# Optimization experiments

Hardware: AMD Instinct MI355X
Metric: run time of the kernel (lower is better)

Reference implementation:

```python
import jax, jax.numpy as jnp
import numpy as np
import math

CHANNELS = 512
OUT_CHANNELS = 512
N_HEADS = 8
WINDOW = 4
K_CH = CHANNELS // N_HEADS


def _conv1x1(x, W, b):
    # x: (B, C_in, T), W: (C_out, C_in), b: (C_out,)
    return jnp.einsum('oc,bct->bot', W, x) + b[None, :, None]


def _get_relative_embeddings(emb, length, window=WINDOW):
    # emb: (H, 2*window+1, k_ch) -> (H, 2*length-1, k_ch)
    pad_length = max(length - (window + 1), 0)
    start = max(window + 1 - length, 0)
    e = jnp.pad(emb, ((0, 0), (pad_length, pad_length), (0, 0))) if pad_length > 0 else emb
    return e[:, start:start + 2 * length - 1]


def _relative_to_absolute(x):
    # x: (B, H, L, 2L-1) -> (B, H, L, L)
    b, h, L, _ = x.shape
    x = jnp.pad(x, ((0, 0), (0, 0), (0, 0), (0, 1)))          # (B,H,L,2L)
    xf = x.reshape(b, h, L * 2 * L)
    xf = jnp.pad(xf, ((0, 0), (0, 0), (L - 1, 0)))
    return xf.reshape(b, h, L + 1, 2 * L - 1)[:, :, :L, L - 1:]


def _absolute_to_relative(x):
    # x: (B, H, L, L) -> (B, H, L, 2L-1)
    b, h, L, _ = x.shape
    x = jnp.pad(x, ((0, 0), (0, 0), (0, 0), (0, L - 1)))       # (B,H,L,2L-1)
    xf = x.reshape(b, h, L * (2 * L - 1))
    xf = jnp.pad(xf, ((0, 0), (0, 0), (L, 0)))
    return xf.reshape(b, h, L, 2 * L)[:, :, :, 1:]


def setup_inputs() -> dict:
    key = jax.random.key(0)
    ks = jax.random.split(key, 16)
    B, C, T = 4, CHANNELS, 1024
    xavier = math.sqrt(2.0 / (C + C))
    rel_std = K_CH ** -0.5
    return {
        'x_q': jax.random.normal(ks[0], (B, C, T), jnp.float32),
        'x_k': jax.random.normal(ks[1], (B, C, T), jnp.float32),
        'x_v': jax.random.normal(ks[2], (B, C, T), jnp.float32),
        'Wq': jax.random.normal(ks[3], (C, C), jnp.float32) * xavier,
        'bq': jnp.zeros((C,), jnp.float32),
        'Wk': jax.random.normal(ks[4], (C, C), jnp.float32) * xavier,
        'bk': jnp.zeros((C,), jnp.float32),
        'Wv': jax.random.normal(ks[5], (C, C), jnp.float32) * xavier,
        'bv': jnp.zeros((C,), jnp.float32),
        'Wo': jax.random.normal(ks[6], (OUT_CHANNELS, C), jnp.float32) * xavier,
        'bo': jnp.zeros((OUT_CHANNELS,), jnp.float32),
        'emb_rel_k': jax.random.normal(ks[7], (N_HEADS, 2 * WINDOW + 1, K_CH), jnp.float32) * rel_std,
        'emb_rel_v': jax.random.normal(ks[8], (N_HEADS, 2 * WINDOW + 1, K_CH), jnp.float32) * rel_std,
    }


def reference(x_q, x_k, x_v, Wq, bq, Wk, bk, Wv, bv, Wo, bo, emb_rel_k, emb_rel_v):
    q = _conv1x1(x_q, Wq, bq)
    k = _conv1x1(x_k, Wk, bk)
    v = _conv1x1(x_v, Wv, bv)
    B, C, T = q.shape
    # (B, C, T) -> (B, H, T, k_ch); head h owns contiguous k_ch channel chunk
    qh = q.reshape(B, N_HEADS, K_CH, T).transpose(0, 1, 3, 2) / math.sqrt(K_CH)
    kh = k.reshape(B, N_HEADS, K_CH, T).transpose(0, 1, 3, 2)
    vh = v.reshape(B, N_HEADS, K_CH, T).transpose(0, 1, 3, 2)
    scores = jnp.einsum('bhtd,bhsd->bhts', qh, kh)              # (B,H,T,T)
    rel_k = _get_relative_embeddings(emb_rel_k, T)              # (H,2T-1,d)
    rel_logits = jnp.einsum('bhtd,hmd->bhtm', qh, rel_k)        # (B,H,T,2T-1)
    scores = scores + _relative_to_absolute(rel_logits)
    attn = jax.nn.softmax(scores, axis=-1)
    ctx = jnp.einsum('bhts,bhsd->bhtd', attn, vh)
    rel_w = _absolute_to_relative(attn)                         # (B,H,T,2T-1)
    rel_v = _get_relative_embeddings(emb_rel_v, T)
    ctx = ctx + jnp.einsum('bhtm,hmd->bhtd', rel_w, rel_v)
    out = ctx.transpose(0, 1, 3, 2).reshape(B, C, T)
    return _conv1x1(out, Wo, bo)
```

## Files before the change

kernel.cpp:

```cpp
#include <hip/hip_runtime.h>

#define T_LEN 1024
#define NH 8
#define DH 64
#define CCH 512
#define LOG2E 1.44269504088896340736f

typedef _Float16 f16;
typedef _Float16 f16x8 __attribute__((ext_vector_type(8)));
typedef _Float16 f16x4 __attribute__((ext_vector_type(4)));
typedef float f32x4 __attribute__((ext_vector_type(4)));

__global__ __launch_bounds__(256)
void xpose_fp16(const float* __restrict__ x0, const float* __restrict__ x1,
                const float* __restrict__ x2, f16* __restrict__ o0,
                f16* __restrict__ o1, f16* __restrict__ o2, int B)
{
    const int t0 = blockIdx.x * 64, c0 = blockIdx.y * 64;
    const int which = blockIdx.z / B, b = blockIdx.z % B;
    const float* x = (which == 0) ? x0 : (which == 1) ? x1 : x2;
    f16* o = (which == 0) ? o0 : (which == 1) ? o1 : o2;

    __shared__ float L[64 * 68];
    const int cl = threadIdx.x & 63, g = threadIdx.x >> 6;
    const float* src = x + ((size_t)(b * CCH + c0 + cl)) * T_LEN + t0 + g * 16;
    #pragma unroll
    for (int j = 0; j < 4; ++j)
        *(float4*)&L[cl * 68 + g * 16 + 4 * j] = *(const float4*)&src[4 * j];
    __syncthreads();
    const int tl = threadIdx.x & 63, cg = (threadIdx.x >> 6) * 16;
    f16 h[16];
    #pragma unroll
    for (int j = 0; j < 16; ++j) h[j] = (f16)L[(cg + j) * 68 + tl];
    f16* dst = o + ((size_t)(b * T_LEN + t0 + tl)) * CCH + c0 + cg;
    *(f16x8*)&dst[0] = *(f16x8*)&h[0];
    *(f16x8*)&dst[8] = *(f16x8*)&h[8];
}

__global__ __launch_bounds__(256)
void wconv(const float* __restrict__ w0, const float* __restrict__ w1,
           const float* __restrict__ w2, const float* __restrict__ w3,
           f16* __restrict__ o0, f16* __restrict__ o1,
           f16* __restrict__ o2, f16* __restrict__ o3)
{
    const int y = blockIdx.y;
    const float* w = (y == 0) ? w0 : (y == 1) ? w1 : (y == 2) ? w2 : w3;
    f16* o = (y == 0) ? o0 : (y == 1) ? o1 : (y == 2) ? o2 : o3;
    const int i = (blockIdx.x * 256 + threadIdx.x) * 4;
    float4 v = *(const float4*)&w[i];
    f16x4 hv = {(f16)v.x, (f16)v.y, (f16)v.z, (f16)v.w};
    *(f16x4*)&o[i] = hv;
}

__global__ __launch_bounds__(256)
void proj_qkv(const f16* __restrict__ xq, const f16* __restrict__ xk,
              const f16* __restrict__ xv, const f16* __restrict__ wq,
              const f16* __restrict__ wk, const f16* __restrict__ wv,
              const float* __restrict__ bq, const float* __restrict__ bk,
              const float* __restrict__ bv, f16* __restrict__ qo,
              f16* __restrict__ ko, f16* __restrict__ vo)
{
    const int which = blockIdx.z;
    const f16* X = (which == 0) ? xq : (which == 1) ? xk : xv;
    const f16* W = (which == 0) ? wq : (which == 1) ? wk : wv;
    const float* bias = (which == 0) ? bq : (which == 1) ? bk : bv;
    const float scale = (which == 0) ? 0.125f * LOG2E : 1.0f;

    const int r0 = blockIdx.x * 64;
    const int o0 = blockIdx.y * 64;
    const int tid = threadIdx.x;
    const int w = tid >> 6, quad = (tid >> 4) & 3, l15 = tid & 15;

    __shared__ f16 Xs[64 * 72], Ws[64 * 72];
    f32x4 acc[4] = {};

    for (int c0 = 0; c0 < CCH; c0 += 64) {
        if (c0) __syncthreads();
        #pragma unroll
        for (int j = 0; j < 2; ++j) {
            int cid = tid + 256 * j;
            int row = cid >> 3, c8 = (cid & 7) * 8;
            *(f16x8*)&Xs[row * 72 + c8] = *(const f16x8*)&X[(size_t)(r0 + row) * CCH + c0 + c8];
            *(f16x8*)&Ws[row * 72 + c8] = *(const f16x8*)&W[(size_t)(o0 + row) * CCH + c0 + c8];
        }
        __syncthreads();
        const f16* Ab = (which < 2) ? Xs : Ws;
        const f16* Bb = (which < 2) ? Ws : Xs;
        #pragma unroll
        for (int ks = 0; ks < 2; ++ks) {
            f16x8 a = *(const f16x8*)&Ab[(16 * w + l15) * 72 + ks * 32 + quad * 8];
            #pragma unroll
            for (int ct = 0; ct < 4; ++ct) {
                f16x8 bf = *(const f16x8*)&Bb[(16 * ct + l15) * 72 + ks * 32 + quad * 8];
                acc[ct] = __builtin_amdgcn_mfma_f32_16x16x32_f16(a, bf, acc[ct], 0, 0, 0);
            }
        }
    }

    if (which < 2) {
        f16* out = (which == 0) ? qo : ko;
        #pragma unroll
        for (int ct = 0; ct < 4; ++ct) {
            int col = o0 + 16 * ct + l15;
            float bvl = bias[col];
            #pragma unroll
            for (int r = 0; r < 4; ++r) {
                int row = r0 + 16 * w + quad * 4 + r;
                out[(size_t)row * CCH + col] = (f16)((acc[ct][r] + bvl) * scale);
            }
        }
    } else {
        const int bb = r0 >> 10, tb = r0 & 1023;
        #pragma unroll
        for (int r = 0; r < 4; ++r) {
            int row_o = o0 + 16 * w + quad * 4 + r;
            float bvl = bias[row_o];
            #pragma unroll
            for (int ct = 0; ct < 4; ++ct)
                vo[((size_t)(bb * CCH + row_o)) * T_LEN + tb + 16 * ct + l15] =
                    (f16)(acc[ct][r] + bvl);
        }
    }
}

__global__ __launch_bounds__(256)
void proj_out(const f16* __restrict__ ctx, const f16* __restrict__ Wo,
              const float* __restrict__ bo, float* __restrict__ out)
{
    const int r0 = blockIdx.x * 64;
    const int o0 = blockIdx.y * 64;
    const int tid = threadIdx.x;
    const int w = tid >> 6, quad = (tid >> 4) & 3, l15 = tid & 15;

    __shared__ f16 Xs[64 * 72], Ws[64 * 72];
    f32x4 acc[4] = {};

    for (int c0 = 0; c0 < CCH; c0 += 64) {
        if (c0) __syncthreads();
        #pragma unroll
        for (int j = 0; j < 2; ++j) {
            int cid = tid + 256 * j;
            int row = cid >> 3, c8 = (cid & 7) * 8;
            *(f16x8*)&Xs[row * 72 + c8] = *(const f16x8*)&ctx[(size_t)(r0 + row) * CCH + c0 + c8];
            *(f16x8*)&Ws[row * 72 + c8] = *(const f16x8*)&Wo[(size_t)(o0 + row) * CCH + c0 + c8];
        }
        __syncthreads();
        #pragma unroll
        for (int ks = 0; ks < 2; ++ks) {
            f16x8 a = *(const f16x8*)&Ws[(16 * w + l15) * 72 + ks * 32 + quad * 8];
            #pragma unroll
            for (int ct = 0; ct < 4; ++ct) {
                f16x8 bf = *(const f16x8*)&Xs[(16 * ct + l15) * 72 + ks * 32 + quad * 8];
                acc[ct] = __builtin_amdgcn_mfma_f32_16x16x32_f16(a, bf, acc[ct], 0, 0, 0);
            }
        }
    }

    const int bb = r0 >> 10, tb = r0 & 1023;
    #pragma unroll
    for (int r = 0; r < 4; ++r) {
        int row_o = o0 + 16 * w + quad * 4 + r;
        float bvl = bo[row_o];
        #pragma unroll
        for (int ct = 0; ct < 4; ++ct)
            out[((size_t)(bb * CCH + row_o)) * T_LEN + tb + 16 * ct + l15] =
                acc[ct][r] + bvl;
    }
}

__global__ __launch_bounds__(256)
void attn_mfma(const f16* __restrict__ q, const f16* __restrict__ k,
               const f16* __restrict__ v, const float* __restrict__ ekg,
               const float* __restrict__ evg, f16* __restrict__ ctx)
{
    const int t0 = blockIdx.x * 64, h = blockIdx.y, b = blockIdx.z;
    const int tid = threadIdx.x;
    const int w = tid >> 6, quad = (tid >> 4) & 3, l15 = tid & 15;

    __shared__ f16 Qs[64 * 72], Ks[64 * 72], Vs[64 * 72], Ps[64 * 72];
    __shared__ float eks[9 * 64], evs[9 * 64];

    for (int i = tid; i < 9 * 64; i += 256) {
        eks[i] = ekg[h * 9 * 64 + i];
        evs[i] = evg[h * 9 * 64 + i];
    }
    #pragma unroll
    for (int j = 0; j < 2; ++j) {
        int cid = tid + 256 * j;
        int row = cid >> 3, c8 = (cid & 7) * 8;
        *(f16x8*)&Qs[row * 72 + c8] =
            *(const f16x8*)&q[((size_t)(b * T_LEN + t0 + row)) * CCH + h * DH + c8];
    }
    __syncthreads();

    float m_run[4], l_run[4];
    f32x4 O[4] = {};
    #pragma unroll
    for (int r = 0; r < 4; ++r) { m_run[r] = -1e30f; l_run[r] = 0.f; }

    const bool corner_hi = (blockIdx.x == 0);
    const bool corner_lo = (blockIdx.x == 15);

    for (int kb = 0; kb < 16; ++kb) {
        const int s0 = kb * 64;
        if (kb) __syncthreads();
        #pragma unroll
        for (int j = 0; j < 2; ++j) {
            int cid = tid + 256 * j;
            int row = cid >> 3, c8 = (cid & 7) * 8;
            *(f16x8*)&Ks[row * 72 + c8] =
                *(const f16x8*)&k[((size_t)(b * T_LEN + s0 + row)) * CCH + h * DH + c8];
            *(f16x8*)&Vs[row * 72 + c8] =
                *(const f16x8*)&v[((size_t)(b * CCH + h * DH + row)) * T_LEN + s0 + c8];
        }
        __syncthreads();

        f32x4 S[4] = {};
        #pragma unroll
        for (int ks = 0; ks < 2; ++ks) {
            f16x8 a = *(const f16x8*)&Qs[(16 * w + l15) * 72 + ks * 32 + quad * 8];
            #pragma unroll
            for (int ct = 0; ct < 4; ++ct) {
                f16x8 bf = *(const f16x8*)&Ks[(16 * ct + l15) * 72 + ks * 32 + quad * 8];
                S[ct] = __builtin_amdgcn_mfma_f32_16x16x32_f16(a, bf, S[ct], 0, 0, 0);
            }
        }

        if ((corner_hi && kb == 15) || (corner_lo && kb == 0)) {
            #pragma unroll
            for (int ct = 0; ct < 4; ++ct)
                #pragma unroll
                for (int r = 0; r < 4; ++r) {
                    int row_l = 16 * w + quad * 4 + r;
                    int df = (s0 + 16 * ct + l15) - (t0 + row_l);
                    if (df >= 1019 && df <= 1023) {
                        const float* ekp = &eks[(df - 1019) * 64];
                        float sacc = 0.f;
                        for (int d = 0; d < 64; ++d)
                            sacc += (float)Qs[row_l * 72 + d] * ekp[d];
                        S[ct][r] += sacc;
                    } else if (df >= -1023 && df <= -1021) {
                        const float* ekp = &eks[(1029 + df) * 64];
                        float sacc = 0.f;
                        for (int d = 0; d < 64; ++d)
                            sacc += (float)Qs[(row_l - 1) * 72 + d] * ekp[d];
                        S[ct][r] += sacc;
                    }
                }
        }

        float alpha[4];
        #pragma unroll
        for (int r = 0; r < 4; ++r) {
            float m = fmaxf(fmaxf(S[0][r], S[1][r]), fmaxf(S[2][r], S[3][r]));
            #pragma unroll
            for (int d = 1; d < 16; d <<= 1) m = fmaxf(m, __shfl_xor(m, d));
            float mn = fmaxf(m_run[r], m);
            alpha[r] = exp2f(m_run[r] - mn);
            m_run[r] = mn;
        }
        #pragma unroll
        for (int r = 0; r < 4; ++r) {
            float p0 = exp2f(S[0][r] - m_run[r]);
            float p1 = exp2f(S[1][r] - m_run[r]);
            float p2 = exp2f(S[2][r] - m_run[r]);
            float p3 = exp2f(S[3][r] - m_run[r]);
            S[0][r] = p0; S[1][r] = p1; S[2][r] = p2; S[3][r] = p3;
            float rs = p0 + p1 + p2 + p3;
            #pragma unroll
            for (int d = 1; d < 16; d <<= 1) rs += __shfl_xor(rs, d);
            l_run[r] = l_run[r] * alpha[r] + rs;
            O[0][r] *= alpha[r]; O[1][r] *= alpha[r];
            O[2][r] *= alpha[r]; O[3][r] *= alpha[r];
        }

        #pragma unroll
        for (int ct = 0; ct < 4; ++ct)
            #pragma unroll
            for (int r = 0; r < 4; ++r)
                Ps[(16 * w + quad * 4 + r) * 72 + 16 * ct + l15] = (f16)S[ct][r];
        __syncthreads();

        #pragma unroll
        for (int ks = 0; ks < 2; ++ks) {
            f16x8 a = *(const f16x8*)&Ps[(16 * w + l15) * 72 + ks * 32 + quad * 8];
            #pragma unroll
            for (int ct = 0; ct < 4; ++ct) {
                f16x8 bf = *(const f16x8*)&Vs[(16 * ct + l15) * 72 + ks * 32 + quad * 8];
                O[ct] = __builtin_amdgcn_mfma_f32_16x16x32_f16(a, bf, O[ct], 0, 0, 0);
            }
        }

        if (s0 <= t0 + 67 && s0 + 63 >= t0 - 4) {
            #pragma unroll
            for (int r = 0; r < 4; ++r) {
                int row_l = 16 * w + quad * 4 + r;
                int t_g = t0 + row_l;
                int slo = max(s0, t_g - 4), shi = min(s0 + 63, t_g + 4);
                for (int s = slo; s <= shi; ++s) {
                    float p = (float)Ps[row_l * 72 + (s - s0)];
                    const float* evp = &evs[(s - t_g + 4) * 64];
                    #pragma unroll
                    for (int ct = 0; ct < 4; ++ct)
                        O[ct][r] += p * evp[16 * ct + l15];
                }
            }
        }
    }

    #pragma unroll
    for (int r = 0; r < 4; ++r) l_run[r] = 1.0f / l_run[r];
    #pragma unroll
    for (int ct = 0; ct < 4; ++ct)
        #pragma unroll
        for (int r = 0; r < 4; ++r) {
            int row = t0 + 16 * w + quad * 4 + r;
            ctx[((size_t)(b * T_LEN + row)) * CCH + h * DH + 16 * ct + l15] =
                (f16)(O[ct][r] * l_run[r]);
        }
}

extern "C" void kernel_launch(void* const* d_in, const int* in_sizes, int n_in,
                              void* d_out, int out_size, void* d_ws, size_t ws_size,
                              hipStream_t stream)
{
    const float* x_q = (const float*)d_in[0];
    const float* x_k = (const float*)d_in[1];
    const float* x_v = (const float*)d_in[2];
    const float* Wq  = (const float*)d_in[3];
    const float* bq  = (const float*)d_in[4];
    const float* Wk  = (const float*)d_in[5];
    const float* bk  = (const float*)d_in[6];
    const float* Wv  = (const float*)d_in[7];
    const float* bv  = (const float*)d_in[8];
    const float* Wo  = (const float*)d_in[9];
    const float* bo  = (const float*)d_in[10];
    const float* erk = (const float*)d_in[11];
    const float* erv = (const float*)d_in[12];

    const int B = in_sizes[0] / (CCH * T_LEN);
    const size_t te = (size_t)B * CCH * T_LEN;
    const size_t we = (size_t)CCH * CCH;

    f16* p = (f16*)d_ws;
    f16* xTq = p; p += te;
    f16* xTk = p; p += te;
    f16* xTv = p; p += te;
    f16* wqh = p; p += we;
    f16* wkh = p; p += we;
    f16* wvh = p; p += we;
    f16* woh = p; p += we;
    f16* qh  = p; p += te;
    f16* kh  = p; p += te;
    f16* vh  = p; p += te;
    f16* ch  = p; p += te;

    dim3 blk(256);
    xpose_fp16<<<dim3(T_LEN / 64, CCH / 64, 3 * B), blk, 0, stream>>>(
        x_q, x_k, x_v, xTq, xTk, xTv, B);
    wconv<<<dim3(256, 4), blk, 0, stream>>>(Wq, Wk, Wv, Wo, wqh, wkh, wvh, woh);
    proj_qkv<<<dim3(B * 16, 8, 3), blk, 0, stream>>>(
        xTq, xTk, xTv, wqh, wkh, wvh, bq, bk, bv, qh, kh, vh);
    attn_mfma<<<dim3(T_LEN / 64, NH, B), blk, 0, stream>>>(qh, kh, vh, erk, erv, ch);
    proj_out<<<dim3(B * 16, 8), blk, 0, stream>>>(ch, woh, bo, (float*)d_out);
}
```

Measured before the change: 171.4 us.

## Split attention over key halves, drop online max, use LDS DMA and swizzle

```diff
diff --git a/kernel.cpp b/kernel.cpp
--- a/kernel.cpp
+++ b/kernel.cpp
@@ -11,45 +11,53 @@
 typedef _Float16 f16x4 __attribute__((ext_vector_type(4)));
 typedef float f32x4 __attribute__((ext_vector_type(4)));
 
+__device__ __forceinline__ void dma16(const void* g, void* l)
+{
+    __builtin_amdgcn_global_load_lds((const __attribute__((address_space(1))) void*)g,
+                                     (__attribute__((address_space(3))) void*)l, 16, 0, 0);
+}
+
 __global__ __launch_bounds__(256)
-void xpose_fp16(const float* __restrict__ x0, const float* __restrict__ x1,
-                const float* __restrict__ x2, f16* __restrict__ o0,
-                f16* __restrict__ o1, f16* __restrict__ o2, int B)
-{
-    const int t0 = blockIdx.x * 64, c0 = blockIdx.y * 64;
-    const int which = blockIdx.z / B, b = blockIdx.z % B;
-    const float* x = (which == 0) ? x0 : (which == 1) ? x1 : x2;
-    f16* o = (which == 0) ? o0 : (which == 1) ? o1 : o2;
-
-    __shared__ float L[64 * 68];
-    const int cl = threadIdx.x & 63, g = threadIdx.x >> 6;
-    const float* src = x + ((size_t)(b * CCH + c0 + cl)) * T_LEN + t0 + g * 16;
-    #pragma unroll
-    for (int j = 0; j < 4; ++j)
-        *(float4*)&L[cl * 68 + g * 16 + 4 * j] = *(const float4*)&src[4 * j];
-    __syncthreads();
-    const int tl = threadIdx.x & 63, cg = (threadIdx.x >> 6) * 16;
-    f16 h[16];
-    #pragma unroll
-    for (int j = 0; j < 16; ++j) h[j] = (f16)L[(cg + j) * 68 + tl];
-    f16* dst = o + ((size_t)(b * T_LEN + t0 + tl)) * CCH + c0 + cg;
-    *(f16x8*)&dst[0] = *(f16x8*)&h[0];
-    *(f16x8*)&dst[8] = *(f16x8*)&h[8];
-}
-
-__global__ __launch_bounds__(256)
-void wconv(const float* __restrict__ w0, const float* __restrict__ w1,
-           const float* __restrict__ w2, const float* __restrict__ w3,
-           f16* __restrict__ o0, f16* __restrict__ o1,
-           f16* __restrict__ o2, f16* __restrict__ o3)
-{
-    const int y = blockIdx.y;
-    const float* w = (y == 0) ? w0 : (y == 1) ? w1 : (y == 2) ? w2 : w3;
-    f16* o = (y == 0) ? o0 : (y == 1) ? o1 : (y == 2) ? o2 : o3;
-    const int i = (blockIdx.x * 256 + threadIdx.x) * 4;
-    float4 v = *(const float4*)&w[i];
-    f16x4 hv = {(f16)v.x, (f16)v.y, (f16)v.z, (f16)v.w};
-    *(f16x4*)&o[i] = hv;
+void prep_kernel(const float* __restrict__ x0, const float* __restrict__ x1,
+                 const float* __restrict__ x2, const float* __restrict__ W0,
+                 const float* __restrict__ W1, const float* __restrict__ W2,
+                 const float* __restrict__ W3, f16* __restrict__ o0,
+                 f16* __restrict__ o1, f16* __restrict__ o2, f16* __restrict__ w0,
+                 f16* __restrict__ w1, f16* __restrict__ w2, f16* __restrict__ w3,
+                 int B)
+{
+    const int z = blockIdx.z;
+    if (z < 3 * B) {
+        const int t0 = blockIdx.x * 64, c0 = blockIdx.y * 64;
+        const int which = z / B, b = z % B;
+        const float* x = (which == 0) ? x0 : (which == 1) ? x1 : x2;
+        f16* o = (which == 0) ? o0 : (which == 1) ? o1 : o2;
+
+        __shared__ float L[64 * 68];
+        const int cl = threadIdx.x & 63, g = threadIdx.x >> 6;
+        const float* src = x + ((size_t)(b * CCH + c0 + cl)) * T_LEN + t0 + g * 16;
+        #pragma unroll
+        for (int j = 0; j < 4; ++j)
+            *(float4*)&L[cl * 68 + g * 16 + 4 * j] = *(const float4*)&src[4 * j];
+        __syncthreads();
+        const int tl = threadIdx.x & 63, cg = (threadIdx.x >> 6) * 16;
+        f16 h[16];
+        #pragma unroll
+        for (int j = 0; j < 16; ++j) h[j] = (f16)L[(cg + j) * 68 + tl];
+        f16* dst = o + ((size_t)(b * T_LEN + t0 + tl)) * CCH + c0 + cg;
+        *(f16x8*)&dst[0] = *(f16x8*)&h[0];
+        *(f16x8*)&dst[8] = *(f16x8*)&h[8];
+    } else {
+        const int slice = z - 3 * B;
+        size_t i = ((size_t)(slice * 128 + blockIdx.y * 16 + blockIdx.x) * 256 + threadIdx.x) * 4;
+        const int wi = (int)(i >> 18);
+        const size_t off = i & 262143;
+        const float* src = (wi == 0) ? W0 : (wi == 1) ? W1 : (wi == 2) ? W2 : W3;
+        f16* dst = (wi == 0) ? w0 : (wi == 1) ? w1 : (wi == 2) ? w2 : w3;
+        float4 v4 = *(const float4*)&src[off];
+        f16x4 h = {(f16)v4.x, (f16)v4.y, (f16)v4.z, (f16)v4.w};
+        *(f16x4*)&dst[off] = h;
+    }
 }
 
 __global__ __launch_bounds__(256)
@@ -124,8 +132,161 @@
 }
 
 __global__ __launch_bounds__(256)
-void proj_out(const f16* __restrict__ ctx, const f16* __restrict__ Wo,
-              const float* __restrict__ bo, float* __restrict__ out)
+void attn_mfma(const f16* __restrict__ q, const f16* __restrict__ kk,
+               const f16* __restrict__ v, const float* __restrict__ ekg,
+               const float* __restrict__ evg, f16* __restrict__ Op0,
+               f16* __restrict__ Op1, float* __restrict__ l0,
+               float* __restrict__ l1)
+{
+    const int t0 = blockIdx.x * 64, h = blockIdx.y;
+    const int b = blockIdx.z >> 1, split = blockIdx.z & 1;
+    const int tid = threadIdx.x;
+    const int w = tid >> 6, lane = tid & 63;
+    const int quad = lane >> 4, l15 = lane & 15;
+
+    f16* Op = split ? Op1 : Op0;
+    float* lbuf = split ? l1 : l0;
+
+    __shared__ __align__(16) f16 Qs[4096], Ks[4096], Vs[4096], Ps[4096];
+    __shared__ float eks[576], evs[576];
+
+    const int srow = tid >> 3;
+    const int scol = ((tid & 7) ^ (srow & 7)) << 3;
+
+    for (int i = tid; i < 576; i += 256) {
+        eks[i] = ekg[h * 576 + i];
+        evs[i] = evg[h * 576 + i];
+    }
+
+    dma16(q + ((size_t)(b * T_LEN + t0 + srow)) * CCH + h * DH + scol, &Qs[(size_t)tid * 8]);
+    dma16(q + ((size_t)(b * T_LEN + t0 + srow + 32)) * CCH + h * DH + scol, &Qs[((size_t)tid + 256) * 8]);
+    __syncthreads();
+
+    f16x8 qf[2];
+    #pragma unroll
+    for (int ks = 0; ks < 2; ++ks)
+        qf[ks] = *(const f16x8*)&Qs[(16 * w + l15) * 64 + (((ks * 4 + quad) ^ (l15 & 7)) << 3)];
+
+    const int kb0 = split * 8;
+    const f16* gk = kk + ((size_t)(b * T_LEN + kb0 * 64 + srow)) * CCH + h * DH + scol;
+    const f16* gv = v + ((size_t)(b * CCH + h * DH + srow)) * T_LEN + kb0 * 64 + scol;
+
+    const int myt = 16 * w + l15;
+    float Ssum = 0.f;
+    f32x4 O[4] = {};
+
+    const bool corner_hi = (blockIdx.x == 0) && (split == 1);
+    const bool corner_lo = (blockIdx.x == 15) && (split == 0);
+
+    for (int kb = kb0; kb < kb0 + 8; ++kb) {
+        __syncthreads();
+        dma16(gk, &Ks[(size_t)tid * 8]);
+        dma16(gk + (size_t)32 * CCH, &Ks[((size_t)tid + 256) * 8]);
+        dma16(gv, &Vs[(size_t)tid * 8]);
+        dma16(gv + (size_t)32 * T_LEN, &Vs[((size_t)tid + 256) * 8]);
+        gk += (size_t)64 * CCH;
+        gv += 64;
+        __syncthreads();
+
+        f32x4 S[4] = {};
+        #pragma unroll
+        for (int ks = 0; ks < 2; ++ks) {
+            #pragma unroll
+            for (int ct = 0; ct < 4; ++ct) {
+                f16x8 a = *(const f16x8*)&Ks[(16 * ct + l15) * 64 + (((ks * 4 + quad) ^ (l15 & 7)) << 3)];
+                S[ct] = __builtin_amdgcn_mfma_f32_16x16x32_f16(a, qf[ks], S[ct], 0, 0, 0);
+            }
+        }
+
+        if ((corner_hi && kb == 15) || (corner_lo && kb == 0)) {
+            const int s0g = kb * 64;
+            #pragma unroll
+            for (int ct = 0; ct < 4; ++ct)
+                #pragma unroll
+                for (int r = 0; r < 4; ++r) {
+                    int t_g = t0 + myt;
+                    int s_g = s0g + 16 * ct + 4 * quad + r;
+                    int df = s_g - t_g;
+                    if (df >= 1019 && df <= 1023) {
+                        const float* ekp = &eks[(df - 1019) * 64];
+                        float sacc = 0.f;
+                        for (int d = 0; d < 64; ++d)
+                            sacc += (float)Qs[myt * 64 + (((d >> 3) ^ (myt & 7)) << 3) + (d & 7)] * ekp[d];
+                        S[ct][r] += sacc;
+                    } else if (df >= -1023 && df <= -1021) {
+                        const float* ekp = &eks[(1029 + df) * 64];
+                        const int t2 = myt - 1;
+                        float sacc = 0.f;
+                        for (int d = 0; d < 64; ++d)
+                            sacc += (float)Qs[t2 * 64 + (((d >> 3) ^ (t2 & 7)) << 3) + (d & 7)] * ekp[d];
+                        S[ct][r] += sacc;
+                    }
+                }
+        }
+
+        #pragma unroll
+        for (int ct = 0; ct < 4; ++ct) {
+            f16x4 pk_;
+            #pragma unroll
+            for (int r = 0; r < 4; ++r) {
+                float p = exp2f(S[ct][r]);
+                Ssum += p;
+                pk_[r] = (f16)p;
+            }
+            int colh = (((2 * ct + (quad >> 1)) ^ (myt & 7)) << 3) + (quad & 1) * 4;
+            *(f16x4*)&Ps[myt * 64 + colh] = pk_;
+        }
+        __syncthreads();
+
+        #pragma unroll
+        for (int ks = 0; ks < 2; ++ks) {
+            f16x8 a = *(const f16x8*)&Ps[(16 * w + l15) * 64 + (((ks * 4 + quad) ^ (l15 & 7)) << 3)];
+            #pragma unroll
+            for (int ct = 0; ct < 4; ++ct) {
+                f16x8 bf = *(const f16x8*)&Vs[(16 * ct + l15) * 64 + (((ks * 4 + quad) ^ (l15 & 7)) << 3)];
+                O[ct] = __builtin_amdgcn_mfma_f32_16x16x32_f16(a, bf, O[ct], 0, 0, 0);
+            }
+        }
+
+        const int s0g = kb * 64;
+        if (s0g <= t0 + 67 && s0g + 63 >= t0 - 4) {
+            #pragma unroll
+            for (int r = 0; r < 4; ++r) {
+                int t_loc = 16 * w + 4 * quad + r;
+                int t_g = t0 + t_loc;
+                int slo = max(s0g, t_g - 4), shi = min(s0g + 63, t_g + 4);
+                for (int s = slo; s <= shi; ++s) {
+                    int sl = s - s0g;
+                    float p = (float)Ps[t_loc * 64 + (((sl >> 3) ^ (t_loc & 7)) << 3) + (sl & 7)];
+                    const float* evp = &evs[(s - t_g + 4) * 64];
+                    #pragma unroll
+                    for (int ct = 0; ct < 4; ++ct)
+                        O[ct][r] += p * evp[16 * ct + l15];
+                }
+            }
+        }
+    }
+
+    Ssum += __shfl_xor(Ssum, 16);
+    Ssum += __shfl_xor(Ssum, 32);
+    if (quad == 0)
+        lbuf[((size_t)b * NH + h) * T_LEN + t0 + myt] = Ssum;
+
+    #pragma unroll
+    for (int r = 0; r < 4; ++r) {
+        int t_g = t0 + 16 * w + 4 * quad + r;
+        size_t rowo = ((size_t)(b * T_LEN + t_g)) * CCH + h * DH;
+        #pragma unroll
+        for (int ct = 0; ct < 4; ++ct)
+            Op[rowo + 16 * ct + l15] = (f16)O[ct][r];
+    }
+}
+
+__global__ __launch_bounds__(256)
+void proj_out(const f16* __restrict__ Op0, const f16* __restrict__ Op1,
+              const float* __restrict__ l0, const float* __restrict__ l1,
+              const f16* __restrict__ Wo, const float* __restrict__ bo,
+              float* __restrict__ out)
 {
     const int r0 = blockIdx.x * 64;
     const int o0 = blockIdx.y * 64;
@@ -140,9 +301,20 @@
         #pragma unroll
         for (int j = 0; j < 2; ++j) {
             int cid = tid + 256 * j;
-            int row = cid >> 3, c8 = (cid & 7) * 8;
-            *(f16x8*)&Xs[row * 72 + c8] = *(const f16x8*)&ctx[(size_t)(r0 + row) * CCH + c0 + c8];
-            *(f16x8*)&Ws[row * 72 + c8] = *(const f16x8*)&Wo[(size_t)(o0 + row) * CCH + c0 + c8];
+            int rw = cid >> 3, cc = (cid & 7) * 8;
+            int gr = r0 + rw;
+            int bb = gr >> 10, tt = gr & 1023;
+            int hh = (c0 + cc) >> 6;
+            size_t li = ((size_t)bb * NH + hh) * T_LEN + tt;
+            float rl = 1.0f / (l0[li] + l1[li]);
+            f16x8 a0 = *(const f16x8*)&Op0[(size_t)gr * CCH + c0 + cc];
+            f16x8 a1 = *(const f16x8*)&Op1[(size_t)gr * CCH + c0 + cc];
+            f16 hx[8];
+            #pragma unroll
+            for (int e = 0; e < 8; ++e)
+                hx[e] = (f16)(((float)a0[e] + (float)a1[e]) * rl);
+            *(f16x8*)&Xs[rw * 72 + cc] = *(f16x8*)hx;
+            *(f16x8*)&Ws[rw * 72 + cc] = *(const f16x8*)&Wo[(size_t)(o0 + rw) * CCH + c0 + cc];
         }
         __syncthreads();
         #pragma unroll
@@ -166,158 +338,6 @@
             out[((size_t)(bb * CCH + row_o)) * T_LEN + tb + 16 * ct + l15] =
                 acc[ct][r] + bvl;
     }
-}
-
-__global__ __launch_bounds__(256)
-void attn_mfma(const f16* __restrict__ q, const f16* __restrict__ k,
-               const f16* __restrict__ v, const float* __restrict__ ekg,
-               const float* __restrict__ evg, f16* __restrict__ ctx)
-{
-    const int t0 = blockIdx.x * 64, h = blockIdx.y, b = blockIdx.z;
-    const int tid = threadIdx.x;
-    const int w = tid >> 6, quad = (tid >> 4) & 3, l15 = tid & 15;
-
-    __shared__ f16 Qs[64 * 72], Ks[64 * 72], Vs[64 * 72], Ps[64 * 72];
-    __shared__ float eks[9 * 64], evs[9 * 64];
-
-    for (int i = tid; i < 9 * 64; i += 256) {
-        eks[i] = ekg[h * 9 * 64 + i];
-        evs[i] = evg[h * 9 * 64 + i];
-    }
-    #pragma unroll
-    for (int j = 0; j < 2; ++j) {
-        int cid = tid + 256 * j;
-        int row = cid >> 3, c8 = (cid & 7) * 8;
-        *(f16x8*)&Qs[row * 72 + c8] =
-            *(const f16x8*)&q[((size_t)(b * T_LEN + t0 + row)) * CCH + h * DH + c8];
-    }
-    __syncthreads();
-
-    float m_run[4], l_run[4];
-    f32x4 O[4] = {};
-    #pragma unroll
-    for (int r = 0; r < 4; ++r) { m_run[r] = -1e30f; l_run[r] = 0.f; }
-
-    const bool corner_hi = (blockIdx.x == 0);
-    const bool corner_lo = (blockIdx.x == 15);
-
-    for (int kb = 0; kb < 16; ++kb) {
-        const int s0 = kb * 64;
-        if (kb) __syncthreads();
-        #pragma unroll
-        for (int j = 0; j < 2; ++j) {
-            int cid = tid + 256 * j;
-            int row = cid >> 3, c8 = (cid & 7) * 8;
-            *(f16x8*)&Ks[row * 72 + c8] =
-                *(const f16x8*)&k[((size_t)(b * T_LEN + s0 + row)) * CCH + h * DH + c8];
-            *(f16x8*)&Vs[row * 72 + c8] =
-                *(const f16x8*)&v[((size_t)(b * CCH + h * DH + row)) * T_LEN + s0 + c8];
-        }
-        __syncthreads();
-
-        f32x4 S[4] = {};
-        #pragma unroll
-        for (int ks = 0; ks < 2; ++ks) {
-            f16x8 a = *(const f16x8*)&Qs[(16 * w + l15) * 72 + ks * 32 + quad * 8];
-            #pragma unroll
-            for (int ct = 0; ct < 4; ++ct) {
-                f16x8 bf = *(const f16x8*)&Ks[(16 * ct + l15) * 72 + ks * 32 + quad * 8];
-                S[ct] = __builtin_amdgcn_mfma_f32_16x16x32_f16(a, bf, S[ct], 0, 0, 0);
-            }
-        }
-
-        if ((corner_hi && kb == 15) || (corner_lo && kb == 0)) {
-            #pragma unroll
-            for (int ct = 0; ct < 4; ++ct)
-                #pragma unroll
-                for (int r = 0; r < 4; ++r) {
-                    int row_l = 16 * w + quad * 4 + r;
-                    int df = (s0 + 16 * ct + l15) - (t0 + row_l);
-                    if (df >= 1019 && df <= 1023) {
-                        const float* ekp = &eks[(df - 1019) * 64];
-                        float sacc = 0.f;
-                        for (int d = 0; d < 64; ++d)
-                            sacc += (float)Qs[row_l * 72 + d] * ekp[d];
-                        S[ct][r] += sacc;
-                    } else if (df >= -1023 && df <= -1021) {
-                        const float* ekp = &eks[(1029 + df) * 64];
-                        float sacc = 0.f;
-                        for (int d = 0; d < 64; ++d)
-                            sacc += (float)Qs[(row_l - 1) * 72 + d] * ekp[d];
-                        S[ct][r] += sacc;
-                    }
-                }
-        }
-
-        float alpha[4];
-        #pragma unroll
-        for (int r = 0; r < 4; ++r) {
-            float m = fmaxf(fmaxf(S[0][r], S[1][r]), fmaxf(S[2][r], S[3][r]));
-            #pragma unroll
-            for (int d = 1; d < 16; d <<= 1) m = fmaxf(m, __shfl_xor(m, d));
-            float mn = fmaxf(m_run[r], m);
-            alpha[r] = exp2f(m_run[r] - mn);
-            m_run[r] = mn;
-        }
-        #pragma unroll
-        for (int r = 0; r < 4; ++r) {
-            float p0 = exp2f(S[0][r] - m_run[r]);
-            float p1 = exp2f(S[1][r] - m_run[r]);
-            float p2 = exp2f(S[2][r] - m_run[r]);
-            float p3 = exp2f(S[3][r] - m_run[r]);
-            S[0][r] = p0; S[1][r] = p1; S[2][r] = p2; S[3][r] = p3;
-            float rs = p0 + p1 + p2 + p3;
-            #pragma unroll
-            for (int d = 1; d < 16; d <<= 1) rs += __shfl_xor(rs, d);
-            l_run[r] = l_run[r] * alpha[r] + rs;
-            O[0][r] *= alpha[r]; O[1][r] *= alpha[r];
-            O[2][r] *= alpha[r]; O[3][r] *= alpha[r];
-        }
-
-        #pragma unroll
-        for (int ct = 0; ct < 4; ++ct)
-            #pragma unroll
-            for (int r = 0; r < 4; ++r)
-                Ps[(16 * w + quad * 4 + r) * 72 + 16 * ct + l15] = (f16)S[ct][r];
-        __syncthreads();
-
-        #pragma unroll
-        for (int ks = 0; ks < 2; ++ks) {
-            f16x8 a = *(const f16x8*)&Ps[(16 * w + l15) * 72 + ks * 32 + quad * 8];
-            #pragma unroll
-            for (int ct = 0; ct < 4; ++ct) {
-                f16x8 bf = *(const f16x8*)&Vs[(16 * ct + l15) * 72 + ks * 32 + quad * 8];
-                O[ct] = __builtin_amdgcn_mfma_f32_16x16x32_f16(a, bf, O[ct], 0, 0, 0);
-            }
-        }
-
-        if (s0 <= t0 + 67 && s0 + 63 >= t0 - 4) {
-            #pragma unroll
-            for (int r = 0; r < 4; ++r) {
-                int row_l = 16 * w + quad * 4 + r;
-                int t_g = t0 + row_l;
-                int slo = max(s0, t_g - 4), shi = min(s0 + 63, t_g + 4);
-                for (int s = slo; s <= shi; ++s) {
-                    float p = (float)Ps[row_l * 72 + (s - s0)];
-                    const float* evp = &evs[(s - t_g + 4) * 64];
-                    #pragma unroll
-                    for (int ct = 0; ct < 4; ++ct)
-                        O[ct][r] += p * evp[16 * ct + l15];
-                }
-            }
-        }
-    }
-
-    #pragma unroll
-    for (int r = 0; r < 4; ++r) l_run[r] = 1.0f / l_run[r];
-    #pragma unroll
-    for (int ct = 0; ct < 4; ++ct)
-        #pragma unroll
-        for (int r = 0; r < 4; ++r) {
-            int row = t0 + 16 * w + quad * 4 + r;
-            ctx[((size_t)(b * T_LEN + row)) * CCH + h * DH + 16 * ct + l15] =
-                (f16)(O[ct][r] * l_run[r]);
-        }
 }
 
 extern "C" void kernel_launch(void* const* d_in, const int* in_sizes, int n_in,
@@ -353,14 +373,19 @@
     f16* qh  = p; p += te;
     f16* kh  = p; p += te;
     f16* vh  = p; p += te;
-    f16* ch  = p; p += te;
+
+    f16* Op0 = xTq;
+    f16* Op1 = xTk;
+    float* l0 = (float*)xTv;
+    float* l1 = l0 + (size_t)B * NH * T_LEN;
 
     dim3 blk(256);
-    xpose_fp16<<<dim3(T_LEN / 64, CCH / 64, 3 * B), blk, 0, stream>>>(
-        x_q, x_k, x_v, xTq, xTk, xTv, B);
-    wconv<<<dim3(256, 4), blk, 0, stream>>>(Wq, Wk, Wv, Wo, wqh, wkh, wvh, woh);
+    prep_kernel<<<dim3(16, 8, 3 * B + 8), blk, 0, stream>>>(
+        x_q, x_k, x_v, Wq, Wk, Wv, Wo, xTq, xTk, xTv, wqh, wkh, wvh, woh, B);
     proj_qkv<<<dim3(B * 16, 8, 3), blk, 0, stream>>>(
         xTq, xTk, xTv, wqh, wkh, wvh, bq, bk, bv, qh, kh, vh);
-    attn_mfma<<<dim3(T_LEN / 64, NH, B), blk, 0, stream>>>(qh, kh, vh, erk, erv, ch);
-    proj_out<<<dim3(B * 16, 8), blk, 0, stream>>>(ch, woh, bo, (float*)d_out);
-}
+    attn_mfma<<<dim3(T_LEN / 64, NH, 2 * B), blk, 0, stream>>>(
+        qh, kh, vh, erk, erv, Op0, Op1, l0, l1);
+    proj_out<<<dim3(B * 16, 8), blk, 0, stream>>>(
+        Op0, Op1, l0, l1, woh, bo, (float*)d_out);
+}
```

Measured after the change: 166.4 us. 1.03x faster.
